# Performance work log

Hardware: AMD Instinct MI355X
Metric: run time of the kernel (lower is better)

Reference implementation:

```python
import jax, jax.numpy as jnp
import numpy as np

N_NODES = 100000
N_EDGES = 3200000
F_IN = 128
HID = 32
N_CLASSES = 40
NEG_SLOPE = 0.2


def _add_self_loops(edge_index, n):
    loops = jnp.arange(n, dtype=edge_index.dtype)
    src = jnp.concatenate([edge_index[0], loops])
    dst = jnp.concatenate([edge_index[1], loops])
    return src, dst


def _gat_layer(x, src, dst, W, a_src, a_dst, b, n):
    # h: [N, C]
    h = x @ W
    hs = h[src]                      # [E, C] gathered source features
    alpha_s = hs @ a_src             # [E]
    alpha_d = (h @ a_dst)[dst]       # [E]
    e = jax.nn.leaky_relu(alpha_s + alpha_d, NEG_SLOPE)
    # segment softmax over incoming edges per destination node
    m = jax.ops.segment_max(e, dst, num_segments=n)
    ex = jnp.exp(e - m[dst])
    denom = jax.ops.segment_sum(ex, dst, num_segments=n)
    alpha = ex / denom[dst]
    out = jax.ops.segment_sum(alpha[:, None] * hs, dst, num_segments=n)
    return out + b


def setup_inputs() -> dict:
    key = jax.random.key(0)
    ks = jax.random.split(key, 8)
    x = jax.random.normal(ks[0], (N_NODES, F_IN), dtype=jnp.float32)
    edge_index = jax.random.randint(ks[1], (2, N_EDGES), 0, N_NODES, dtype=jnp.int32)
    W1 = jax.random.normal(ks[2], (F_IN, HID), dtype=jnp.float32) * (1.0 / np.sqrt(F_IN))
    att_src1 = jax.random.normal(ks[3], (HID,), dtype=jnp.float32) * 0.1
    att_dst1 = jax.random.normal(ks[4], (HID,), dtype=jnp.float32) * 0.1
    b1 = jnp.zeros((HID,), dtype=jnp.float32)
    W2 = jax.random.normal(ks[5], (HID, N_CLASSES), dtype=jnp.float32) * (1.0 / np.sqrt(HID))
    att_src2 = jax.random.normal(ks[6], (N_CLASSES,), dtype=jnp.float32) * 0.1
    att_dst2 = jax.random.normal(ks[7], (N_CLASSES,), dtype=jnp.float32) * 0.1
    b2 = jnp.zeros((N_CLASSES,), dtype=jnp.float32)
    return {"x": x, "edge_index": edge_index, "W1": W1, "att_src1": att_src1,
            "att_dst1": att_dst1, "b1": b1, "W2": W2, "att_src2": att_src2,
            "att_dst2": att_dst2, "b2": b2}


def reference(x, edge_index, W1, att_src1, att_dst1, b1, W2, att_src2, att_dst2, b2):
    n = x.shape[0]
    src, dst = _add_self_loops(edge_index, n)  # PyG GATConv default add_self_loops=True
    h = _gat_layer(x, src, dst, W1, att_src1, att_dst1, b1, n)
    h = jax.nn.relu(h)  # dropout is identity in eval mode
    h = _gat_layer(h, src, dst, W2, att_src2, att_dst2, b2, n)
    h = jax.nn.relu(h)
    return jax.nn.log_softmax(h, axis=1)
```

## Files before the change

### kernel.cpp

```cpp
#include <hip/hip_runtime.h>
#include <hip/hip_bf16.h>
#include <hip/hip_fp16.h>
#include <math.h>

#define N_NODES 100000
#define N_EDGES 3200000
#define ET (N_EDGES + N_NODES)
#define F_IN 128
#define HID 32
#define NCLS 40
#define NEG 0.2f

#define NB 782
#define NBLK 782
#define CHUNK 4096
#define BCAP 6144

__global__ __launch_bounds__(256) void kA_hist(const int* __restrict__ dst,
                                               int* __restrict__ Hm) {
    __shared__ int hist[NB];
    int t = threadIdx.x, k = blockIdx.x;
    for (int i = t; i < NB; i += 256) hist[i] = 0;
    __syncthreads();
    int base = k * CHUNK;
#pragma unroll
    for (int j = 0; j < CHUNK / 256; j++) {
        int e = base + j * 256 + t;
        if (e < N_EDGES) atomicAdd(&hist[dst[e] >> 7], 1);
    }
    __syncthreads();
    for (int i = t; i < NB; i += 256) Hm[i * NBLK + k] = hist[i];
}

__global__ void k_scan_a(const int* __restrict__ in, int* __restrict__ out,
                         int* __restrict__ bsums, int L) {
    __shared__ int sd[256];
    int t = threadIdx.x, b = blockIdx.x;
    int base = b * 1024 + t * 4;
    int v0 = 0, v1 = 0, v2 = 0, v3 = 0;
    if (base     < L) v0 = in[base];
    if (base + 1 < L) v1 = in[base + 1];
    if (base + 2 < L) v2 = in[base + 2];
    if (base + 3 < L) v3 = in[base + 3];
    int ts = v0 + v1 + v2 + v3;
    sd[t] = ts;
    __syncthreads();
    for (int off = 1; off < 256; off <<= 1) {
        int xx = (t >= off) ? sd[t - off] : 0;
        __syncthreads();
        sd[t] += xx;
        __syncthreads();
    }
    int ex = sd[t] - ts;
    if (t == 255) bsums[b] = sd[255];
    if (base     < L) out[base]     = ex;
    if (base + 1 < L) out[base + 1] = ex + v0;
    if (base + 2 < L) out[base + 2] = ex + v0 + v1;
    if (base + 3 < L) out[base + 3] = ex + v0 + v1 + v2;
}

__global__ void k_scan_b(const int* __restrict__ bsums, int* __restrict__ boffs, int nb) {
    __shared__ int sd[256];
    int t = threadIdx.x;
    int base = t * 4;
    int v0 = 0, v1 = 0, v2 = 0, v3 = 0;
    if (base     < nb) v0 = bsums[base];
    if (base + 1 < nb) v1 = bsums[base + 1];
    if (base + 2 < nb) v2 = bsums[base + 2];
    if (base + 3 < nb) v3 = bsums[base + 3];
    int ts = v0 + v1 + v2 + v3;
    sd[t] = ts;
    __syncthreads();
    for (int off = 1; off < 256; off <<= 1) {
        int xx = (t >= off) ? sd[t - off] : 0;
        __syncthreads();
        sd[t] += xx;
        __syncthreads();
    }
    int ex = sd[t] - ts;
    if (base     < nb) boffs[base]     = ex;
    if (base + 1 < nb) boffs[base + 1] = ex + v0;
    if (base + 2 < nb) boffs[base + 2] = ex + v0 + v1;
    if (base + 3 < nb) boffs[base + 3] = ex + v0 + v1 + v2;
}

__global__ void k_scan_c(int* __restrict__ out, const int* __restrict__ boffs, int L) {
    int i = blockIdx.x * 256 + threadIdx.x;
    if (i < L) out[i] += boffs[i >> 10];
}

__global__ __launch_bounds__(256) void kA_scatter(
    const int* __restrict__ src, const int* __restrict__ dst,
    const int* __restrict__ Sx, unsigned int* __restrict__ tmp) {
    __shared__ int hist[NB];
    __shared__ int lofs[NB];
    __shared__ int cur[NB];
    __shared__ int tsum[256];
    __shared__ unsigned int stage[CHUNK];
    __shared__ int gpos[CHUNK];
    int t = threadIdx.x, k = blockIdx.x;
    for (int i = t; i < NB; i += 256) hist[i] = 0;
    __syncthreads();
    int base = k * CHUNK;
    int myd[16], mys[16];
#pragma unroll
    for (int j = 0; j < 16; j++) {
        int e = base + j * 256 + t;
        myd[j] = (e < N_EDGES) ? dst[e] : -1;
        mys[j] = (e < N_EDGES) ? src[e] : 0;
        if (myd[j] >= 0) atomicAdd(&hist[myd[j] >> 7], 1);
    }
    __syncthreads();
    int i0 = 4 * t;
    int h0 = (i0     < NB) ? hist[i0]     : 0;
    int h1 = (i0 + 1 < NB) ? hist[i0 + 1] : 0;
    int h2 = (i0 + 2 < NB) ? hist[i0 + 2] : 0;
    int h3 = (i0 + 3 < NB) ? hist[i0 + 3] : 0;
    int ts = h0 + h1 + h2 + h3;
    tsum[t] = ts;
    __syncthreads();
    for (int off = 1; off < 256; off <<= 1) {
        int xx = (t >= off) ? tsum[t - off] : 0;
        __syncthreads();
        tsum[t] += xx;
        __syncthreads();
    }
    int ex = tsum[t] - ts;
    if (i0     < NB) { lofs[i0]     = ex;                cur[i0]     = 0; }
    if (i0 + 1 < NB) { lofs[i0 + 1] = ex + h0;           cur[i0 + 1] = 0; }
    if (i0 + 2 < NB) { lofs[i0 + 2] = ex + h0 + h1;      cur[i0 + 2] = 0; }
    if (i0 + 3 < NB) { lofs[i0 + 3] = ex + h0 + h1 + h2; cur[i0 + 3] = 0; }
    __syncthreads();
#pragma unroll
    for (int j = 0; j < 16; j++) {
        if (myd[j] >= 0) {
            int bkt = myd[j] >> 7;
            int slot = lofs[bkt] + atomicAdd(&cur[bkt], 1);
            stage[slot] = ((unsigned int)(myd[j] & 127) << 17) | (unsigned int)mys[j];
            gpos[slot] = Sx[bkt * NBLK + k] + (slot - lofs[bkt]);
        }
    }
    __syncthreads();
    int nvalid = min(CHUNK, N_EDGES - base);
    for (int i = t; i < nvalid; i += 256) tmp[gpos[i]] = stage[i];
}

__global__ __launch_bounds__(256) void kB_sort(
    const unsigned int* __restrict__ tmp, const int* __restrict__ Sx,
    int* __restrict__ esrc, int* __restrict__ rs, int* __restrict__ deg) {
    __shared__ unsigned int stage[BCAP];
    __shared__ int ordered[BCAP + 128];
    __shared__ int cnt[128], lofs[128], cur[128], sc[128];
    int t = threadIdx.x, b = blockIdx.x;
    int myBase = Sx[b * NBLK];
    int nextBase = (b == NB - 1) ? N_EDGES : Sx[(b + 1) * NBLK];
    int cntE = nextBase - myBase;
    int nNodes = min(128, N_NODES - b * 128);
    if (t < 128) { cnt[t] = 0; cur[t] = 0; }
    __syncthreads();
    for (int i = t; i < cntE; i += 256) {
        unsigned int p = tmp[myBase + i];
        stage[i] = p;
        atomicAdd(&cnt[p >> 17], 1);
    }
    __syncthreads();
    int val = 0;
    if (t < 128) { val = (t < nNodes) ? cnt[t] + 1 : 0; sc[t] = val; }
    __syncthreads();
    for (int off = 1; off < 128; off <<= 1) {
        int xx = 0;
        if (t < 128 && t >= off) xx = sc[t - off];
        __syncthreads();
        if (t < 128) sc[t] += xx;
        __syncthreads();
    }
    if (t < 128) lofs[t] = sc[t] - val;
    __syncthreads();
    if (t < nNodes) ordered[lofs[t]] = b * 128 + t;
    for (int i = t; i < cntE; i += 256) {
        unsigned int p = stage[i];
        int n = p >> 17;
        int slot = lofs[n] + 1 + atomicAdd(&cur[n], 1);
        ordered[slot] = (int)(p & 0x1FFFF);
    }
    __syncthreads();
    int gb = myBase + b * 128;
    int totOut = cntE + nNodes;
    for (int i = t; i < totOut; i += 256) esrc[gb + i] = ordered[i];
    if (t < nNodes) {
        rs[b * 128 + t] = gb + lofs[t];
        deg[b * 128 + t] = cnt[t] + 1;
    }
}

__global__ void k_prep(const float* __restrict__ W2, const float* __restrict__ as2,
                       const float* __restrict__ ad2,
                       float* __restrict__ va_s, float* __restrict__ va_d) {
    int k = threadIdx.x;
    if (k < HID) {
        float ps = 0.f, pd = 0.f;
        for (int c = 0; c < NCLS; c++) {
            float w = W2[k * NCLS + c];
            ps = fmaf(w, as2[c], ps);
            pd = fmaf(w, ad2[c], pd);
        }
        va_s[k] = ps;
        va_d[k] = pd;
    }
}

__global__ __launch_bounds__(256) void k_gemm1(
    const float* __restrict__ x, const float* __restrict__ W1,
    const float* __restrict__ a_s, const float* __restrict__ a_d,
    __half* __restrict__ h1h, float* __restrict__ s1, float* __restrict__ d1) {
    __shared__ float Ws[F_IN * HID];
    __shared__ float xs[8 * F_IN];
    int t = threadIdx.x;
    const float4* W4 = (const float4*)W1;
    float4* Ws4 = (float4*)Ws;
#pragma unroll
    for (int i = 0; i < F_IN * HID / 4 / 256; i++)
        Ws4[t + i * 256] = W4[t + i * 256];
    ((float4*)xs)[t] = ((const float4*)(x + (size_t)blockIdx.x * 8 * F_IN))[t];
    __syncthreads();
    int c = t & 31, g = t >> 5;
    int v = blockIdx.x * 8 + g;
    const float4* xg4 = (const float4*)(xs + g * F_IN);
    float acc = 0.f;
#pragma unroll
    for (int k4 = 0; k4 < F_IN / 4; k4++) {
        float4 xv = xg4[k4];
        int k = k4 * 4;
        acc = fmaf(xv.x, Ws[(k + 0) * HID + c], acc);
        acc = fmaf(xv.y, Ws[(k + 1) * HID + c], acc);
        acc = fmaf(xv.z, Ws[(k + 2) * HID + c], acc);
        acc = fmaf(xv.w, Ws[(k + 3) * HID + c], acc);
    }
    h1h[(size_t)v * HID + c] = __float2half(acc);
    float p = acc * a_s[c];
    float q = acc * a_d[c];
    for (int mm = 16; mm >= 1; mm >>= 1) {
        p += __shfl_xor(p, mm, 32);
        q += __shfl_xor(q, mm, 32);
    }
    if (c == 0) { s1[v] = p; d1[v] = q; }
}

#define GATHER_BODY(SARR, TABLE)                                                  \
    float a0 = 0.f, a1 = 0.f, a2 = 0.f, a3 = 0.f,                                 \
          a4 = 0.f, a5 = 0.f, a6 = 0.f, a7 = 0.f;                                 \
    float den = 0.f;                                                              \
    int t = 0;                                                                    \
    for (; t + 16 <= cnt; t += 16) {                                              \
        int p0 = start + t + e;                                                   \
        int sa0 = esrc[p0];                                                       \
        int sa1 = esrc[p0 + 4];                                                   \
        int sa2 = esrc[p0 + 8];                                                   \
        int sa3 = esrc[p0 + 12];                                                  \
        float sv0 = SARR[sa0];                                                    \
        float sv1 = SARR[sa1];                                                    \
        float sv2 = SARR[sa2];                                                    \
        float sv3 = SARR[sa3];                                                    \
        uint4 hv0 = TABLE[(size_t)sa0 * 4 + q];                                   \
        uint4 hv1 = TABLE[(size_t)sa1 * 4 + q];                                   \
        uint4 hv2 = TABLE[(size_t)sa2 * 4 + q];                                   \
        uint4 hv3 = TABLE[(size_t)sa3 * 4 + q];                                   \
        float e0 = sv0 + dval; e0 = (e0 >= 0.f) ? e0 : NEG * e0;                  \
        float e1 = sv1 + dval; e1 = (e1 >= 0.f) ? e1 : NEG * e1;                  \
        float e2 = sv2 + dval; e2 = (e2 >= 0.f) ? e2 : NEG * e2;                  \
        float e3 = sv3 + dval; e3 = (e3 >= 0.f) ? e3 : NEG * e3;                  \
        float w0 = __expf(e0);                                                    \
        float w1 = __expf(e1);                                                    \
        float w2 = __expf(e2);                                                    \
        float w3 = __expf(e3);                                                    \
        den += (w0 + w1) + (w2 + w3);                                             \
        ACC8(w0, hv0); ACC8(w1, hv1); ACC8(w2, hv2); ACC8(w3, hv3);               \
    }                                                                             \
    for (; t < cnt; t += 4) {                                                     \
        int idx = t + e;                                                          \
        int sa = 0;                                                               \
        float w = 0.f;                                                            \
        if (idx < cnt) {                                                          \
            sa = esrc[start + idx];                                               \
            float ev = SARR[sa] + dval;                                           \
            ev = (ev >= 0.f) ? ev : NEG * ev;                                     \
            w = __expf(ev);                                                       \
        }                                                                         \
        uint4 hv = TABLE[(size_t)sa * 4 + q];                                     \
        ACC8(w, hv);                                                              \
        den += w;                                                                 \
    }

#define ACC8(W, HV)                                                               \
    {                                                                             \
        float2 f0 = __half22float2(*(const __half2*)&(HV).x);                     \
        float2 f1 = __half22float2(*(const __half2*)&(HV).y);                     \
        float2 f2 = __half22float2(*(const __half2*)&(HV).z);                     \
        float2 f3 = __half22float2(*(const __half2*)&(HV).w);                     \
        a0 = fmaf((W), f0.x, a0); a1 = fmaf((W), f0.y, a1);                       \
        a2 = fmaf((W), f1.x, a2); a3 = fmaf((W), f1.y, a3);                       \
        a4 = fmaf((W), f2.x, a4); a5 = fmaf((W), f2.y, a5);                       \
        a6 = fmaf((W), f3.x, a6); a7 = fmaf((W), f3.y, a7);                       \
    }

__global__ __launch_bounds__(256) void k_fused1(
    const int* __restrict__ rs, const int* __restrict__ deg, const int* __restrict__ esrc,
    const uint4* __restrict__ h1r, const float* __restrict__ s1, const float* __restrict__ d1,
    const float* __restrict__ b1, const float* __restrict__ va_s, const float* __restrict__ va_d,
    uint4* __restrict__ hrr, float* __restrict__ s2, float* __restrict__ d2) {
    int tid = threadIdx.x;
    int sub = tid & 15;
    int q = sub & 3;
    int e = sub >> 2;
    int v = blockIdx.x * 16 + (tid >> 4);
    int start = rs[v];
    int cnt = deg[v];
    float dval = d1[v];
    GATHER_BODY(s1, h1r)
#pragma unroll
    for (int off = 4; off <= 8; off <<= 1) {
        a0 += __shfl_xor(a0, off); a1 += __shfl_xor(a1, off);
        a2 += __shfl_xor(a2, off); a3 += __shfl_xor(a3, off);
        a4 += __shfl_xor(a4, off); a5 += __shfl_xor(a5, off);
        a6 += __shfl_xor(a6, off); a7 += __shfl_xor(a7, off);
        den += __shfl_xor(den, off);
    }
    if (e == 0) {
        float iden = 1.f / den;
        const float4* b4 = (const float4*)(b1 + q * 8);
        float4 bA = b4[0], bB = b4[1];
        float o0 = fmaxf(a0 * iden + bA.x, 0.f);
        float o1 = fmaxf(a1 * iden + bA.y, 0.f);
        float o2 = fmaxf(a2 * iden + bA.z, 0.f);
        float o3 = fmaxf(a3 * iden + bA.w, 0.f);
        float o4 = fmaxf(a4 * iden + bB.x, 0.f);
        float o5 = fmaxf(a5 * iden + bB.y, 0.f);
        float o6 = fmaxf(a6 * iden + bB.z, 0.f);
        float o7 = fmaxf(a7 * iden + bB.w, 0.f);
        __half2 p0 = __floats2half2_rn(o0, o1);
        __half2 p1 = __floats2half2_rn(o2, o3);
        __half2 p2 = __floats2half2_rn(o4, o5);
        __half2 p3 = __floats2half2_rn(o6, o7);
        uint4 ov;
        ov.x = *(const unsigned int*)&p0;
        ov.y = *(const unsigned int*)&p1;
        ov.z = *(const unsigned int*)&p2;
        ov.w = *(const unsigned int*)&p3;
        hrr[(size_t)v * 4 + q] = ov;
        const float4* vs4 = (const float4*)(va_s + q * 8);
        const float4* vd4 = (const float4*)(va_d + q * 8);
        float4 sA = vs4[0], sB = vs4[1], dA = vd4[0], dB = vd4[1];
        float ps = o0 * sA.x + o1 * sA.y + o2 * sA.z + o3 * sA.w
                 + o4 * sB.x + o5 * sB.y + o6 * sB.z + o7 * sB.w;
        float pd = o0 * dA.x + o1 * dA.y + o2 * dA.z + o3 * dA.w
                 + o4 * dB.x + o5 * dB.y + o6 * dB.z + o7 * dB.w;
        ps += __shfl_xor(ps, 1); pd += __shfl_xor(pd, 1);
        ps += __shfl_xor(ps, 2); pd += __shfl_xor(pd, 2);
        if (q == 0) { s2[v] = ps; d2[v] = pd; }
    }
}

__global__ __launch_bounds__(256) void k_fused2(
    const int* __restrict__ rs, const int* __restrict__ deg, const int* __restrict__ esrc,
    const uint4* __restrict__ hrr, const float* __restrict__ s2, const float* __restrict__ d2,
    const float* __restrict__ W2, const float* __restrict__ b2, float* __restrict__ out) {
    __shared__ float W2s[HID * NCLS];
    __shared__ float hragg[16][HID];
    __shared__ float zbuf[16][NCLS];
    __shared__ float gm[16], gl[16];
    int tid = threadIdx.x;
    for (int i = tid; i < HID * NCLS; i += 256) W2s[i] = W2[i];
    int sub = tid & 15;
    int q = sub & 3;
    int e = sub >> 2;
    int node = tid >> 4;
    int v = blockIdx.x * 16 + node;
    int start = rs[v];
    int cnt = deg[v];
    float dval = d2[v];
    GATHER_BODY(s2, hrr)
#pragma unroll
    for (int off = 4; off <= 8; off <<= 1) {
        a0 += __shfl_xor(a0, off); a1 += __shfl_xor(a1, off);
        a2 += __shfl_xor(a2, off); a3 += __shfl_xor(a3, off);
        a4 += __shfl_xor(a4, off); a5 += __shfl_xor(a5, off);
        a6 += __shfl_xor(a6, off); a7 += __shfl_xor(a7, off);
        den += __shfl_xor(den, off);
    }
    if (e == 0) {
        float iden = 1.f / den;
        int cb = q * 8;
        hragg[node][cb + 0] = a0 * iden;
        hragg[node][cb + 1] = a1 * iden;
        hragg[node][cb + 2] = a2 * iden;
        hragg[node][cb + 3] = a3 * iden;
        hragg[node][cb + 4] = a4 * iden;
        hragg[node][cb + 5] = a5 * iden;
        hragg[node][cb + 6] = a6 * iden;
        hragg[node][cb + 7] = a7 * iden;
    }
    __syncthreads();
    for (int oi = tid; oi < 16 * NCLS; oi += 256) {
        int n = oi / NCLS, c = oi % NCLS;
        float z = 0.f;
#pragma unroll
        for (int k = 0; k < HID; k++)
            z = fmaf(hragg[n][k], W2s[k * NCLS + c], z);
        zbuf[n][c] = fmaxf(z + b2[c], 0.f);
    }
    __syncthreads();
    if (tid < 16) {
        float mx = -INFINITY;
        for (int c = 0; c < NCLS; c++) mx = fmaxf(mx, zbuf[tid][c]);
        float se = 0.f;
        for (int c = 0; c < NCLS; c++) se += __expf(zbuf[tid][c] - mx);
        gm[tid] = mx;
        gl[tid] = logf(se);
    }
    __syncthreads();
    for (int oi = tid; oi < 16 * NCLS; oi += 256) {
        int n = oi / NCLS, c = oi % NCLS;
        out[(size_t)(blockIdx.x * 16 + n) * NCLS + c] = zbuf[n][c] - gm[n] - gl[n];
    }
}


extern "C" void kernel_launch(void* const* d_in, const int* in_sizes, int n_in,
                              void* d_out, int out_size, void* d_ws, size_t ws_size,
                              hipStream_t stream) {
    (void)in_sizes; (void)n_in; (void)out_size; (void)ws_size;
    const float* x   = (const float*)d_in[0];
    const int*   ei  = (const int*)d_in[1];
    const float* W1  = (const float*)d_in[2];
    const float* as1 = (const float*)d_in[3];
    const float* ad1 = (const float*)d_in[4];
    const float* b1  = (const float*)d_in[5];
    const float* W2  = (const float*)d_in[6];
    const float* as2 = (const float*)d_in[7];
    const float* ad2 = (const float*)d_in[8];
    const float* b2  = (const float*)d_in[9];
    float* out = (float*)d_out;
    const int* srcA = ei;
    const int* dstA = ei + N_EDGES;

    char* w = (char*)d_ws;
    size_t off = 0;
    auto alloc = [&](size_t bytes) {
        char* p = w + off;
        off = (off + bytes + 255) & ~(size_t)255;
        return p;
    };
    int* esrc     = (int*)alloc((size_t)ET * 4);
    int* rs       = (int*)alloc((size_t)N_NODES * 4);
    int* deg      = (int*)alloc((size_t)N_NODES * 4);
    char* region1 = alloc((size_t)N_NODES * HID * 4);
    float* s1     = (float*)alloc((size_t)N_NODES * 4);
    float* d1     = (float*)alloc((size_t)N_NODES * 4);
    char* region2 = alloc((size_t)N_EDGES * 4 + 1024);
    float* s2     = (float*)alloc((size_t)N_NODES * 4);
    float* d2     = (float*)alloc((size_t)N_NODES * 4);
    float* va_s   = (float*)alloc(HID * 4);
    float* va_d   = (float*)alloc(HID * 4);
    int* bsums    = (int*)alloc(1024 * 4);
    int* boffs    = (int*)alloc(1024 * 4);

    const int L = NB * NBLK;
    int* Hm = (int*)region1;
    int* Sx = Hm + ((L + 63) & ~63);
    __half* h1h = (__half*)region1;
    unsigned int* tmp = (unsigned int*)region2;
    __half* hrt = (__half*)region2;

    int nb1 = (L + 1023) / 1024;
    hipLaunchKernelGGL(kA_hist, dim3(NBLK), dim3(256), 0, stream, dstA, Hm);
    hipLaunchKernelGGL(k_scan_a, dim3(nb1), dim3(256), 0, stream, Hm, Sx, bsums, L);
    hipLaunchKernelGGL(k_scan_b, dim3(1), dim3(256), 0, stream, bsums, boffs, nb1);
    hipLaunchKernelGGL(k_scan_c, dim3((L + 255) / 256), dim3(256), 0, stream, Sx, boffs, L);
    hipLaunchKernelGGL(kA_scatter, dim3(NBLK), dim3(256), 0, stream, srcA, dstA, Sx, tmp);
    hipLaunchKernelGGL(kB_sort, dim3(NB), dim3(256), 0, stream, tmp, Sx, esrc, rs, deg);

    hipLaunchKernelGGL(k_prep, dim3(1), dim3(64), 0, stream, W2, as2, ad2, va_s, va_d);
    hipLaunchKernelGGL(k_gemm1, dim3(N_NODES / 8), dim3(256), 0, stream, x, W1, as1, ad1, h1h, s1, d1);
    hipLaunchKernelGGL(k_fused1, dim3(N_NODES / 16), dim3(256), 0, stream, rs, deg, esrc,
                       (const uint4*)h1h, s1, d1, b1, va_s, va_d,
                       (uint4*)hrt, s2, d2);
    hipLaunchKernelGGL(k_fused2, dim3(N_NODES / 16), dim3(256), 0, stream, rs, deg, esrc,
                       (const uint4*)hrt, s2, d2, W2, b2, out);
}
```

Measured before the change: 327.2 us.

## Replace two-pass bucketed CSR sort with atomic count-scan-scatter build

Replaces the multi-kernel bucket histogram, three-stage scan, scatter and per-bucket local sort with a simpler CSR build: global atomic degree counting, a single-block scan, and an atomic-slot scatter of sources. It also folds the W2·att precompute into an extra block of the first GEMM, pads a shared array to avoid bank conflicts, and parallelizes the per-row log-softmax over four lanes with shuffles. The aim is fewer launches and less intermediate traffic. The trade-offs are heavy global atomic contention, a serial single-block scan over all nodes, and a non-deterministic neighbor order within each row, which can change floating-point summation order.

```diff
diff --git a/kernel.cpp b/kernel.cpp
--- a/kernel.cpp
+++ b/kernel.cpp
@@ -10,212 +10,87 @@
 #define HID 32
 #define NCLS 40
 #define NEG 0.2f
-
-#define NB 782
-#define NBLK 782
-#define CHUNK 4096
-#define BCAP 6144
-
-__global__ __launch_bounds__(256) void kA_hist(const int* __restrict__ dst,
-                                               int* __restrict__ Hm) {
-    __shared__ int hist[NB];
-    int t = threadIdx.x, k = blockIdx.x;
-    for (int i = t; i < NB; i += 256) hist[i] = 0;
-    __syncthreads();
-    int base = k * CHUNK;
-#pragma unroll
-    for (int j = 0; j < CHUNK / 256; j++) {
-        int e = base + j * 256 + t;
-        if (e < N_EDGES) atomicAdd(&hist[dst[e] >> 7], 1);
-    }
-    __syncthreads();
-    for (int i = t; i < NB; i += 256) Hm[i * NBLK + k] = hist[i];
-}
-
-__global__ void k_scan_a(const int* __restrict__ in, int* __restrict__ out,
-                         int* __restrict__ bsums, int L) {
-    __shared__ int sd[256];
-    int t = threadIdx.x, b = blockIdx.x;
-    int base = b * 1024 + t * 4;
-    int v0 = 0, v1 = 0, v2 = 0, v3 = 0;
-    if (base     < L) v0 = in[base];
-    if (base + 1 < L) v1 = in[base + 1];
-    if (base + 2 < L) v2 = in[base + 2];
-    if (base + 3 < L) v3 = in[base + 3];
-    int ts = v0 + v1 + v2 + v3;
-    sd[t] = ts;
-    __syncthreads();
-    for (int off = 1; off < 256; off <<= 1) {
-        int xx = (t >= off) ? sd[t - off] : 0;
+#define GEMM_BLKS (N_NODES / 8)
+
+
+__global__ __launch_bounds__(256) void k_cnt(const int* __restrict__ dst,
+                                             int* __restrict__ cnt) {
+    int i = blockIdx.x * 256 + threadIdx.x;
+    int4 d = ((const int4*)dst)[i];
+    atomicAdd(&cnt[d.x], 1);
+    atomicAdd(&cnt[d.y], 1);
+    atomicAdd(&cnt[d.z], 1);
+    atomicAdd(&cnt[d.w], 1);
+}
+
+__global__ __launch_bounds__(1024) void k_scan(const int* __restrict__ cnt,
+                                               int* __restrict__ rs,
+                                               int* __restrict__ deg) {
+    __shared__ int sums[1024];
+    int t = threadIdx.x;
+    const int C = (N_NODES + 1023) / 1024;
+    int lo = t * C, hi = min(lo + C, N_NODES);
+    int s = 0;
+    for (int i = lo; i < hi; i++) s += cnt[i] + 1;
+    sums[t] = s;
+    __syncthreads();
+    for (int off = 1; off < 1024; off <<= 1) {
+        int x = (t >= off) ? sums[t - off] : 0;
         __syncthreads();
-        sd[t] += xx;
+        sums[t] += x;
         __syncthreads();
     }
-    int ex = sd[t] - ts;
-    if (t == 255) bsums[b] = sd[255];
-    if (base     < L) out[base]     = ex;
-    if (base + 1 < L) out[base + 1] = ex + v0;
-    if (base + 2 < L) out[base + 2] = ex + v0 + v1;
-    if (base + 3 < L) out[base + 3] = ex + v0 + v1 + v2;
-}
-
-__global__ void k_scan_b(const int* __restrict__ bsums, int* __restrict__ boffs, int nb) {
-    __shared__ int sd[256];
-    int t = threadIdx.x;
-    int base = t * 4;
-    int v0 = 0, v1 = 0, v2 = 0, v3 = 0;
-    if (base     < nb) v0 = bsums[base];
-    if (base + 1 < nb) v1 = bsums[base + 1];
-    if (base + 2 < nb) v2 = bsums[base + 2];
-    if (base + 3 < nb) v3 = bsums[base + 3];
-    int ts = v0 + v1 + v2 + v3;
-    sd[t] = ts;
-    __syncthreads();
-    for (int off = 1; off < 256; off <<= 1) {
-        int xx = (t >= off) ? sd[t - off] : 0;
-        __syncthreads();
-        sd[t] += xx;
-        __syncthreads();
-    }
-    int ex = sd[t] - ts;
-    if (base     < nb) boffs[base]     = ex;
-    if (base + 1 < nb) boffs[base + 1] = ex + v0;
-    if (base + 2 < nb) boffs[base + 2] = ex + v0 + v1;
-    if (base + 3 < nb) boffs[base + 3] = ex + v0 + v1 + v2;
-}
-
-__global__ void k_scan_c(int* __restrict__ out, const int* __restrict__ boffs, int L) {
-    int i = blockIdx.x * 256 + threadIdx.x;
-    if (i < L) out[i] += boffs[i >> 10];
-}
-
-__global__ __launch_bounds__(256) void kA_scatter(
-    const int* __restrict__ src, const int* __restrict__ dst,
-    const int* __restrict__ Sx, unsigned int* __restrict__ tmp) {
-    __shared__ int hist[NB];
-    __shared__ int lofs[NB];
-    __shared__ int cur[NB];
-    __shared__ int tsum[256];
-    __shared__ unsigned int stage[CHUNK];
-    __shared__ int gpos[CHUNK];
-    int t = threadIdx.x, k = blockIdx.x;
-    for (int i = t; i < NB; i += 256) hist[i] = 0;
-    __syncthreads();
-    int base = k * CHUNK;
-    int myd[16], mys[16];
-#pragma unroll
-    for (int j = 0; j < 16; j++) {
-        int e = base + j * 256 + t;
-        myd[j] = (e < N_EDGES) ? dst[e] : -1;
-        mys[j] = (e < N_EDGES) ? src[e] : 0;
-        if (myd[j] >= 0) atomicAdd(&hist[myd[j] >> 7], 1);
-    }
-    __syncthreads();
-    int i0 = 4 * t;
-    int h0 = (i0     < NB) ? hist[i0]     : 0;
-    int h1 = (i0 + 1 < NB) ? hist[i0 + 1] : 0;
-    int h2 = (i0 + 2 < NB) ? hist[i0 + 2] : 0;
-    int h3 = (i0 + 3 < NB) ? hist[i0 + 3] : 0;
-    int ts = h0 + h1 + h2 + h3;
-    tsum[t] = ts;
-    __syncthreads();
-    for (int off = 1; off < 256; off <<= 1) {
-        int xx = (t >= off) ? tsum[t - off] : 0;
-        __syncthreads();
-        tsum[t] += xx;
-        __syncthreads();
-    }
-    int ex = tsum[t] - ts;
-    if (i0     < NB) { lofs[i0]     = ex;                cur[i0]     = 0; }
-    if (i0 + 1 < NB) { lofs[i0 + 1] = ex + h0;           cur[i0 + 1] = 0; }
-    if (i0 + 2 < NB) { lofs[i0 + 2] = ex + h0 + h1;      cur[i0 + 2] = 0; }
-    if (i0 + 3 < NB) { lofs[i0 + 3] = ex + h0 + h1 + h2; cur[i0 + 3] = 0; }
-    __syncthreads();
-#pragma unroll
-    for (int j = 0; j < 16; j++) {
-        if (myd[j] >= 0) {
-            int bkt = myd[j] >> 7;
-            int slot = lofs[bkt] + atomicAdd(&cur[bkt], 1);
-            stage[slot] = ((unsigned int)(myd[j] & 127) << 17) | (unsigned int)mys[j];
-            gpos[slot] = Sx[bkt * NBLK + k] + (slot - lofs[bkt]);
-        }
-    }
-    __syncthreads();
-    int nvalid = min(CHUNK, N_EDGES - base);
-    for (int i = t; i < nvalid; i += 256) tmp[gpos[i]] = stage[i];
-}
-
-__global__ __launch_bounds__(256) void kB_sort(
-    const unsigned int* __restrict__ tmp, const int* __restrict__ Sx,
-    int* __restrict__ esrc, int* __restrict__ rs, int* __restrict__ deg) {
-    __shared__ unsigned int stage[BCAP];
-    __shared__ int ordered[BCAP + 128];
-    __shared__ int cnt[128], lofs[128], cur[128], sc[128];
-    int t = threadIdx.x, b = blockIdx.x;
-    int myBase = Sx[b * NBLK];
-    int nextBase = (b == NB - 1) ? N_EDGES : Sx[(b + 1) * NBLK];
-    int cntE = nextBase - myBase;
-    int nNodes = min(128, N_NODES - b * 128);
-    if (t < 128) { cnt[t] = 0; cur[t] = 0; }
-    __syncthreads();
-    for (int i = t; i < cntE; i += 256) {
-        unsigned int p = tmp[myBase + i];
-        stage[i] = p;
-        atomicAdd(&cnt[p >> 17], 1);
-    }
-    __syncthreads();
-    int val = 0;
-    if (t < 128) { val = (t < nNodes) ? cnt[t] + 1 : 0; sc[t] = val; }
-    __syncthreads();
-    for (int off = 1; off < 128; off <<= 1) {
-        int xx = 0;
-        if (t < 128 && t >= off) xx = sc[t - off];
-        __syncthreads();
-        if (t < 128) sc[t] += xx;
-        __syncthreads();
-    }
-    if (t < 128) lofs[t] = sc[t] - val;
-    __syncthreads();
-    if (t < nNodes) ordered[lofs[t]] = b * 128 + t;
-    for (int i = t; i < cntE; i += 256) {
-        unsigned int p = stage[i];
-        int n = p >> 17;
-        int slot = lofs[n] + 1 + atomicAdd(&cur[n], 1);
-        ordered[slot] = (int)(p & 0x1FFFF);
-    }
-    __syncthreads();
-    int gb = myBase + b * 128;
-    int totOut = cntE + nNodes;
-    for (int i = t; i < totOut; i += 256) esrc[gb + i] = ordered[i];
-    if (t < nNodes) {
-        rs[b * 128 + t] = gb + lofs[t];
-        deg[b * 128 + t] = cnt[t] + 1;
-    }
-}
-
-__global__ void k_prep(const float* __restrict__ W2, const float* __restrict__ as2,
-                       const float* __restrict__ ad2,
-                       float* __restrict__ va_s, float* __restrict__ va_d) {
-    int k = threadIdx.x;
-    if (k < HID) {
-        float ps = 0.f, pd = 0.f;
-        for (int c = 0; c < NCLS; c++) {
-            float w = W2[k * NCLS + c];
-            ps = fmaf(w, as2[c], ps);
-            pd = fmaf(w, ad2[c], pd);
-        }
-        va_s[k] = ps;
-        va_d[k] = pd;
+    int run = sums[t] - s;
+    for (int i = lo; i < hi; i++) {
+        int c = cnt[i] + 1;
+        rs[i] = run;
+        deg[i] = c;
+        run += c;
+    }
+}
+
+__global__ __launch_bounds__(256) void k_scat(const int* __restrict__ src,
+                                              const int* __restrict__ dst,
+                                              const int* __restrict__ rs,
+                                              int* __restrict__ cur,
+                                              int* __restrict__ esrc) {
+    const int EB = N_EDGES / 4 / 256;
+    if (blockIdx.x < EB) {
+        int i = blockIdx.x * 256 + threadIdx.x;
+        int4 s4 = ((const int4*)src)[i];
+        int4 d4 = ((const int4*)dst)[i];
+        esrc[rs[d4.x] + 1 + atomicAdd(&cur[d4.x], 1)] = s4.x;
+        esrc[rs[d4.y] + 1 + atomicAdd(&cur[d4.y], 1)] = s4.y;
+        esrc[rs[d4.z] + 1 + atomicAdd(&cur[d4.z], 1)] = s4.z;
+        esrc[rs[d4.w] + 1 + atomicAdd(&cur[d4.w], 1)] = s4.w;
+    } else {
+        int v = (blockIdx.x - EB) * 256 + threadIdx.x;
+        if (v < N_NODES) esrc[rs[v]] = v;
     }
 }
 
 __global__ __launch_bounds__(256) void k_gemm1(
     const float* __restrict__ x, const float* __restrict__ W1,
     const float* __restrict__ a_s, const float* __restrict__ a_d,
-    __half* __restrict__ h1h, float* __restrict__ s1, float* __restrict__ d1) {
+    __half* __restrict__ h1h, float* __restrict__ s1, float* __restrict__ d1,
+    const float* __restrict__ W2, const float* __restrict__ as2,
+    const float* __restrict__ ad2, float* __restrict__ va_s, float* __restrict__ va_d) {
     __shared__ float Ws[F_IN * HID];
     __shared__ float xs[8 * F_IN];
     int t = threadIdx.x;
+    if (blockIdx.x == GEMM_BLKS) {
+        if (t < HID) {
+            float ps = 0.f, pd = 0.f;
+            for (int c = 0; c < NCLS; c++) {
+                float w = W2[t * NCLS + c];
+                ps = fmaf(w, as2[c], ps);
+                pd = fmaf(w, ad2[c], pd);
+            }
+            va_s[t] = ps;
+            va_d[t] = pd;
+        }
+        return;
+    }
     const float4* W4 = (const float4*)W1;
     float4* Ws4 = (float4*)Ws;
 #pragma unroll
@@ -365,7 +240,7 @@
     const uint4* __restrict__ hrr, const float* __restrict__ s2, const float* __restrict__ d2,
     const float* __restrict__ W2, const float* __restrict__ b2, float* __restrict__ out) {
     __shared__ float W2s[HID * NCLS];
-    __shared__ float hragg[16][HID];
+    __shared__ float hragg[16][HID + 1];
     __shared__ float zbuf[16][NCLS];
     __shared__ float gm[16], gl[16];
     int tid = threadIdx.x;
@@ -409,13 +284,17 @@
         zbuf[n][c] = fmaxf(z + b2[c], 0.f);
     }
     __syncthreads();
-    if (tid < 16) {
-        float mx = -INFINITY;
-        for (int c = 0; c < NCLS; c++) mx = fmaxf(mx, zbuf[tid][c]);
+    if (tid < 64) {
+        int n = tid >> 2, j = tid & 3;
+        float mx = 0.f;
+        for (int c = j; c < NCLS; c += 4) mx = fmaxf(mx, zbuf[n][c]);
+        mx = fmaxf(mx, __shfl_xor(mx, 1));
+        mx = fmaxf(mx, __shfl_xor(mx, 2));
         float se = 0.f;
-        for (int c = 0; c < NCLS; c++) se += __expf(zbuf[tid][c] - mx);
-        gm[tid] = mx;
-        gl[tid] = logf(se);
+        for (int c = j; c < NCLS; c += 4) se += __expf(zbuf[n][c] - mx);
+        se += __shfl_xor(se, 1);
+        se += __shfl_xor(se, 2);
+        if (j == 0) { gm[n] = mx; gl[n] = logf(se); }
     }
     __syncthreads();
     for (int oi = tid; oi < 16 * NCLS; oi += 256) {
@@ -453,34 +332,25 @@
     int* esrc     = (int*)alloc((size_t)ET * 4);
     int* rs       = (int*)alloc((size_t)N_NODES * 4);
     int* deg      = (int*)alloc((size_t)N_NODES * 4);
-    char* region1 = alloc((size_t)N_NODES * HID * 4);
+    int* cntcur   = (int*)alloc((size_t)2 * N_NODES * 4);
+    __half* h1h   = (__half*)alloc((size_t)N_NODES * HID * 2);
     float* s1     = (float*)alloc((size_t)N_NODES * 4);
     float* d1     = (float*)alloc((size_t)N_NODES * 4);
-    char* region2 = alloc((size_t)N_EDGES * 4 + 1024);
+    __half* hrt   = (__half*)alloc((size_t)N_NODES * HID * 2);
     float* s2     = (float*)alloc((size_t)N_NODES * 4);
     float* d2     = (float*)alloc((size_t)N_NODES * 4);
     float* va_s   = (float*)alloc(HID * 4);
     float* va_d   = (float*)alloc(HID * 4);
-    int* bsums    = (int*)alloc(1024 * 4);
-    int* boffs    = (int*)alloc(1024 * 4);
-
-    const int L = NB * NBLK;
-    int* Hm = (int*)region1;
-    int* Sx = Hm + ((L + 63) & ~63);
-    __half* h1h = (__half*)region1;
-    unsigned int* tmp = (unsigned int*)region2;
-    __half* hrt = (__half*)region2;
-
-    int nb1 = (L + 1023) / 1024;
-    hipLaunchKernelGGL(kA_hist, dim3(NBLK), dim3(256), 0, stream, dstA, Hm);
-    hipLaunchKernelGGL(k_scan_a, dim3(nb1), dim3(256), 0, stream, Hm, Sx, bsums, L);
-    hipLaunchKernelGGL(k_scan_b, dim3(1), dim3(256), 0, stream, bsums, boffs, nb1);
-    hipLaunchKernelGGL(k_scan_c, dim3((L + 255) / 256), dim3(256), 0, stream, Sx, boffs, L);
-    hipLaunchKernelGGL(kA_scatter, dim3(NBLK), dim3(256), 0, stream, srcA, dstA, Sx, tmp);
-    hipLaunchKernelGGL(kB_sort, dim3(NB), dim3(256), 0, stream, tmp, Sx, esrc, rs, deg);
-
-    hipLaunchKernelGGL(k_prep, dim3(1), dim3(64), 0, stream, W2, as2, ad2, va_s, va_d);
-    hipLaunchKernelGGL(k_gemm1, dim3(N_NODES / 8), dim3(256), 0, stream, x, W1, as1, ad1, h1h, s1, d1);
+    int* cnt = cntcur;
+    int* cur = cntcur + N_NODES;
+
+    hipMemsetAsync(cntcur, 0, (size_t)2 * N_NODES * 4, stream);
+    hipLaunchKernelGGL(k_cnt, dim3(N_EDGES / 4 / 256), dim3(256), 0, stream, dstA, cnt);
+    hipLaunchKernelGGL(k_scan, dim3(1), dim3(1024), 0, stream, cnt, rs, deg);
+    hipLaunchKernelGGL(k_scat, dim3(N_EDGES / 4 / 256 + (N_NODES + 255) / 256), dim3(256),
+                       0, stream, srcA, dstA, rs, cur, esrc);
+    hipLaunchKernelGGL(k_gemm1, dim3(GEMM_BLKS + 1), dim3(256), 0, stream, x, W1, as1, ad1,
+                       h1h, s1, d1, W2, as2, ad2, va_s, va_d);
     hipLaunchKernelGGL(k_fused1, dim3(N_NODES / 16), dim3(256), 0, stream, rs, deg, esrc,
                        (const uint4*)h1h, s1, d1, b1, va_s, va_d,
                        (uint4*)hrt, s2, d2);
```

Measured after the change: 788.7 us. +141.0%, slower.
